# Kernel optimization log

Hardware: AMD Instinct MI355X
Metric: run time of the kernel (lower is better)

Reference implementation:

```python
import jax, jax.numpy as jnp
import numpy as np
from jax import lax

B, C, HID, H, W = 8, 256, 64, 64, 64

def conv3x3(x, w, b):
    # x: [B,C_in,H,W], w: [C_out,C_in,3,3], b: [C_out]
    y = lax.conv_general_dilated(x, w, window_strides=(1, 1), padding='SAME',
                                 dimension_numbers=('NCHW', 'OIHW', 'NCHW'))
    return y + b[None, :, None, None]

def setup_inputs() -> dict:
    key = jax.random.key(0)
    ks = jax.random.split(key, 7)
    s_in = 1.0 / np.sqrt(C * 9)
    return {
        'x': jax.random.normal(ks[0], (B, C, H, W), dtype=jnp.float32),
        'Wq': jax.random.normal(ks[1], (HID, C, 3, 3), dtype=jnp.float32) * s_in,
        'bq': jax.random.normal(ks[2], (HID,), dtype=jnp.float32) * s_in,
        'Wk': jax.random.normal(ks[3], (HID, C, 3, 3), dtype=jnp.float32) * s_in,
        'bk': jax.random.normal(ks[4], (HID,), dtype=jnp.float32) * s_in,
        'Wv': jax.random.normal(ks[5], (C, C, 3, 3), dtype=jnp.float32) * s_in,
        'bv': jax.random.normal(ks[6], (C,), dtype=jnp.float32) * s_in,
    }

def reference(x, Wq, bq, Wk, bk, Wv, bv):
    b, c, w, h = x.shape
    n = w * h
    q = conv3x3(x, Wq, bq).reshape(b, -1, n).transpose(0, 2, 1)  # [B,N,hid]
    k = conv3x3(x, Wk, bk).reshape(b, -1, n)                      # [B,hid,N]
    v = conv3x3(x, Wv, bv).reshape(b, c, n)                       # [B,C,N]
    attn = jax.nn.softmax(jnp.einsum('bnd,bdm->bnm', q, k), axis=-1)  # [B,N,N]
    # out = bmm(value, attn^T): out[b,c,m] = sum_n v[b,c,n] * attn[b,m,n]
    out = jnp.einsum('bcn,bmn->bcm', v, attn).reshape(b, c, w, h)
    # F.interpolate(out, h, mode='bilinear') with H==W is an exact identity
    return out + x
```

## Files before the change

kernel.cpp:

```cpp
#include <hip/hip_runtime.h>
#include <math.h>

#define NB   8
#define NC   256
#define ND   64
#define NPIX 4096
#define LSTR 72

typedef short bf16x8 __attribute__((ext_vector_type(8)));
typedef float f32x4  __attribute__((ext_vector_type(4)));
typedef float f32x16 __attribute__((ext_vector_type(16)));

static __device__ __forceinline__ ushort f2bf(float f) {
    uint u = __float_as_uint(f);
    u += 0x7fffu + ((u >> 16) & 1u);
    return (ushort)(u >> 16);
}
static __device__ __forceinline__ float bf2f(ushort h) {
    return __uint_as_float(((uint)h) << 16);
}

__global__ __launch_bounds__(256) void transpose_x(
    const float* __restrict__ x, ushort* __restrict__ xth, ushort* __restrict__ xtl)
{
    __shared__ float tile[64][68];
    const int t = threadIdx.x;
    const int p0 = blockIdx.x * 64, c0 = blockIdx.y * 64, b = blockIdx.z;

    const int cl = t >> 4, p4 = (t & 15) * 4;
    #pragma unroll
    for (int i = 0; i < 4; i++) {
        const int c = cl + 16 * i;
        *(float4*)&tile[c][p4] =
            *(const float4*)&x[((size_t)(b * NC + c0 + c)) * NPIX + p0 + p4];
    }
    __syncthreads();

    const int pl = t & 63, ch = t >> 6;
    float v[16];
    #pragma unroll
    for (int j = 0; j < 16; j++) v[j] = tile[ch * 16 + j][pl];
    ushort h[16], l[16];
    #pragma unroll
    for (int j = 0; j < 16; j++) {
        h[j] = f2bf(v[j]);
        l[j] = f2bf(v[j] - bf2f(h[j]));
    }
    const size_t o = ((size_t)(b * NPIX + p0 + pl)) * 256 + c0 + ch * 16;
    *(uint4*)&xth[o]     = *(uint4*)&h[0];
    *(uint4*)&xth[o + 8] = *(uint4*)&h[8];
    *(uint4*)&xtl[o]     = *(uint4*)&l[0];
    *(uint4*)&xtl[o + 8] = *(uint4*)&l[8];
}

__global__ __launch_bounds__(256) void transpose_w(
    const float* __restrict__ Wq, const float* __restrict__ Wk,
    const float* __restrict__ Wv,
    ushort* __restrict__ qh, ushort* __restrict__ ql,
    ushort* __restrict__ kh, ushort* __restrict__ kl,
    ushort* __restrict__ vh)
{
    __shared__ float wb[2304];
    const int g = blockIdx.x, t = threadIdx.x;
    const float* src;
    ushort *dh, *dl;
    int co, Co, split;
    if (g < 64)       { src = Wq + (size_t)g * 2304; co = g;       Co = 64;  dh = qh; dl = ql; split = 1; }
    else if (g < 128) { src = Wk + (size_t)(g - 64) * 2304; co = g - 64; Co = 64; dh = kh; dl = kl; split = 1; }
    else              { src = Wv + (size_t)(g - 128) * 2304; co = g - 128; Co = 256; dh = vh; dl = nullptr; split = 0; }

    for (int i = t; i < 2304; i += 256) wb[i] = src[i];
    __syncthreads();
    for (int j = t; j < 2304; j += 256) {
        const int rs = j >> 8, ci = j & 255;
        const float v = wb[ci * 9 + rs];
        const ushort hv = f2bf(v);
        const size_t o = ((size_t)(rs * Co + co)) * 256 + ci;
        dh[o] = hv;
        if (split) dl[o] = f2bf(v - bf2f(hv));
    }
}

__global__ __launch_bounds__(256) void conv_split_k(
    const ushort* __restrict__ xth, const ushort* __restrict__ xtl,
    const ushort* __restrict__ wqh, const ushort* __restrict__ wql,
    const ushort* __restrict__ wkh, const ushort* __restrict__ wkl,
    const float* __restrict__ bq, const float* __restrict__ bk,
    ushort* __restrict__ qoh, ushort* __restrict__ qol,
    ushort* __restrict__ koh, ushort* __restrict__ kol)
{
    extern __shared__ char smem[];
    ushort* xsh = (ushort*)smem;
    ushort* xsl = xsh + 6 * 66 * 24;
    ushort* wsp = xsl + 6 * 66 * 24;
    float*  sbias = (float*)(wsp + 9 * 64 * 24);

    const int hq = blockIdx.x, b = blockIdx.y, ct = blockIdx.z;
    const ushort* wth = ct ? wkh : wqh;
    const ushort* wtl = ct ? wkl : wql;
    const float*  bias = ct ? bk : bq;
    ushort* outh = ct ? koh : qoh;
    ushort* outl = ct ? kol : qol;

    const int t = threadIdx.x;
    const int wv = t >> 6, lane = t & 63;
    const int l31 = lane & 31, khl = lane >> 5;
    const int lanebase = l31 * 24 + khl * 8;
    const int h = hq * 4 + wv;

    if (t < 64) sbias[t] = bias[t];
    for (int i = t; i < 384; i += 256) {
        const int p = i / 192, r2 = i % 192;
        const int row = r2 / 32, e = (r2 % 32) / 16, ci = r2 & 15;
        (p ? xsl : xsh)[(row * 66 + e * 65) * 24 + ci] = 0;
    }

    f32x16 a00 = {0}, a01 = {0}, a10 = {0}, a11 = {0};

    for (int ch = 0; ch < 16; ch++) {
        __syncthreads();
        const int ci0 = ch * 16;
        #pragma unroll
        for (int pl2 = 0; pl2 < 2; pl2++) {
            const ushort* src = pl2 ? xtl : xth;
            ushort* dst = pl2 ? xsl : xsh;
            #pragma unroll
            for (int i = 0; i < 3; i++) {
                const int a = i * 256 + t;
                const int cih = a & 1, col = (a >> 1) & 63, row = a >> 7;
                const int hs = hq * 4 + row - 1;
                uint4 val = {0, 0, 0, 0};
                if (hs >= 0 && hs < 64)
                    val = *(const uint4*)&src[((size_t)(b * NPIX + hs * 64 + col)) * 256 + ci0 + cih * 8];
                *(uint4*)&dst[(row * 66 + 1 + col) * 24 + cih * 8] = val;
            }
        }
        #pragma unroll
        for (int i = 0; i < 5; i++) {
            const int a = i * 256 + t;
            if (a < 1152) {
                const int cih = a & 1, co = (a >> 1) & 63, rs = a >> 7;
                uint4 wv4 = *(const uint4*)&wth[((size_t)(rs * 64 + co)) * 256 + ci0 + cih * 8];
                *(uint4*)&wsp[(rs * 64 + co) * 24 + cih * 8] = wv4;
            }
        }
        __syncthreads();
        #pragma unroll
        for (int rs = 0; rs < 9; rs++) {
            const int r = rs / 3, s = rs % 3;
            bf16x8 A0 = *(const bf16x8*)&wsp[rs * 1536 + lanebase];
            bf16x8 A1 = *(const bf16x8*)&wsp[rs * 1536 + 768 + lanebase];
            const int xo = ((wv + r) * 66 + s) * 24 + lanebase;
            bf16x8 B0h = *(const bf16x8*)&xsh[xo];
            bf16x8 B1h = *(const bf16x8*)&xsh[xo + 768];
            bf16x8 B0l = *(const bf16x8*)&xsl[xo];
            bf16x8 B1l = *(const bf16x8*)&xsl[xo + 768];
            a00 = __builtin_amdgcn_mfma_f32_32x32x16_bf16(A0, B0h, a00, 0, 0, 0);
            a01 = __builtin_amdgcn_mfma_f32_32x32x16_bf16(A0, B1h, a01, 0, 0, 0);
            a10 = __builtin_amdgcn_mfma_f32_32x32x16_bf16(A1, B0h, a10, 0, 0, 0);
            a11 = __builtin_amdgcn_mfma_f32_32x32x16_bf16(A1, B1h, a11, 0, 0, 0);
            a00 = __builtin_amdgcn_mfma_f32_32x32x16_bf16(A0, B0l, a00, 0, 0, 0);
            a01 = __builtin_amdgcn_mfma_f32_32x32x16_bf16(A0, B1l, a01, 0, 0, 0);
            a10 = __builtin_amdgcn_mfma_f32_32x32x16_bf16(A1, B0l, a10, 0, 0, 0);
            a11 = __builtin_amdgcn_mfma_f32_32x32x16_bf16(A1, B1l, a11, 0, 0, 0);
        }
        __syncthreads();
        #pragma unroll
        for (int i = 0; i < 5; i++) {
            const int a = i * 256 + t;
            if (a < 1152) {
                const int cih = a & 1, co = (a >> 1) & 63, rs = a >> 7;
                uint4 wv4 = *(const uint4*)&wtl[((size_t)(rs * 64 + co)) * 256 + ci0 + cih * 8];
                *(uint4*)&wsp[(rs * 64 + co) * 24 + cih * 8] = wv4;
            }
        }
        __syncthreads();
        #pragma unroll
        for (int rs = 0; rs < 9; rs++) {
            const int r = rs / 3, s = rs % 3;
            bf16x8 A0 = *(const bf16x8*)&wsp[rs * 1536 + lanebase];
            bf16x8 A1 = *(const bf16x8*)&wsp[rs * 1536 + 768 + lanebase];
            const int xo = ((wv + r) * 66 + s) * 24 + lanebase;
            bf16x8 B0h = *(const bf16x8*)&xsh[xo];
            bf16x8 B1h = *(const bf16x8*)&xsh[xo + 768];
            a00 = __builtin_amdgcn_mfma_f32_32x32x16_bf16(A0, B0h, a00, 0, 0, 0);
            a01 = __builtin_amdgcn_mfma_f32_32x32x16_bf16(A0, B1h, a01, 0, 0, 0);
            a10 = __builtin_amdgcn_mfma_f32_32x32x16_bf16(A1, B0h, a10, 0, 0, 0);
            a11 = __builtin_amdgcn_mfma_f32_32x32x16_bf16(A1, B1h, a11, 0, 0, 0);
        }
    }

    const float4* sb4 = (const float4*)sbias;
    #pragma unroll
    for (int ms = 0; ms < 2; ms++)
        #pragma unroll
        for (int ns = 0; ns < 2; ns++) {
            const f32x16 av = ms ? (ns ? a11 : a10) : (ns ? a01 : a00);
            const int p = h * 64 + ns * 32 + l31;
            #pragma unroll
            for (int g = 0; g < 4; g++) {
                const float4 bi = sb4[ms * 8 + 2 * g + khl];
                float v0 = av[4 * g + 0] + bi.x;
                float v1 = av[4 * g + 1] + bi.y;
                float v2 = av[4 * g + 2] + bi.z;
                float v3 = av[4 * g + 3] + bi.w;
                ushort4 hv, lv;
                hv.x = f2bf(v0); lv.x = f2bf(v0 - bf2f(hv.x));
                hv.y = f2bf(v1); lv.y = f2bf(v1 - bf2f(hv.y));
                hv.z = f2bf(v2); lv.z = f2bf(v2 - bf2f(hv.z));
                hv.w = f2bf(v3); lv.w = f2bf(v3 - bf2f(hv.w));
                const size_t o = ((size_t)(b * NPIX + p)) * 64 + ms * 32 + 8 * g + 4 * khl;
                *(ushort4*)&outh[o] = hv;
                *(ushort4*)&outl[o] = lv;
            }
        }
}

__global__ __launch_bounds__(256) void conv_v_k(
    const ushort* __restrict__ xth, const ushort* __restrict__ wtv,
    const float* __restrict__ bv, ushort* __restrict__ vout)
{
    extern __shared__ char smem[];
    ushort* xsh = (ushort*)smem;
    ushort* wsp = xsh + 6 * 66 * 24;
    float*  sbias = (float*)(wsp + 9 * 64 * 24);

    const int hq = blockIdx.x, b = blockIdx.y, co0 = blockIdx.z * 64;
    const int t = threadIdx.x;
    const int wv = t >> 6, lane = t & 63;
    const int l31 = lane & 31, khl = lane >> 5;
    const int lanebase = l31 * 24 + khl * 8;
    const int h = hq * 4 + wv;

    if (t < 64) sbias[t] = bv[co0 + t];
    for (int i = t; i < 192; i += 256) {
        const int row = i / 32, e = (i % 32) / 16, ci = i & 15;
        xsh[(row * 66 + e * 65) * 24 + ci] = 0;
    }

    f32x16 a00 = {0}, a01 = {0}, a10 = {0}, a11 = {0};

    for (int ch = 0; ch < 16; ch++) {
        __syncthreads();
        const int ci0 = ch * 16;
        #pragma unroll
        for (int i = 0; i < 3; i++) {
            const int a = i * 256 + t;
            const int cih = a & 1, col = (a >> 1) & 63, row = a >> 7;
            const int hs = hq * 4 + row - 1;
            uint4 val = {0, 0, 0, 0};
            if (hs >= 0 && hs < 64)
                val = *(const uint4*)&xth[((size_t)(b * NPIX + hs * 64 + col)) * 256 + ci0 + cih * 8];
            *(uint4*)&xsh[(row * 66 + 1 + col) * 24 + cih * 8] = val;
        }
        #pragma unroll
        for (int i = 0; i < 5; i++) {
            const int a = i * 256 + t;
            if (a < 1152) {
                const int cih = a & 1, co = (a >> 1) & 63, rs = a >> 7;
                uint4 wv4 = *(const uint4*)&wtv[((size_t)(rs * 256 + co0 + co)) * 256 + ci0 + cih * 8];
                *(uint4*)&wsp[(rs * 64 + co) * 24 + cih * 8] = wv4;
            }
        }
        __syncthreads();
        #pragma unroll
        for (int rs = 0; rs < 9; rs++) {
            const int r = rs / 3, s = rs % 3;
            const int xo = ((wv + r) * 66 + s) * 24 + lanebase;
            bf16x8 A0 = *(const bf16x8*)&xsh[xo];
            bf16x8 A1 = *(const bf16x8*)&xsh[xo + 768];
            bf16x8 B0 = *(const bf16x8*)&wsp[rs * 1536 + lanebase];
            bf16x8 B1 = *(const bf16x8*)&wsp[rs * 1536 + 768 + lanebase];
            a00 = __builtin_amdgcn_mfma_f32_32x32x16_bf16(A0, B0, a00, 0, 0, 0);
            a01 = __builtin_amdgcn_mfma_f32_32x32x16_bf16(A0, B1, a01, 0, 0, 0);
            a10 = __builtin_amdgcn_mfma_f32_32x32x16_bf16(A1, B0, a10, 0, 0, 0);
            a11 = __builtin_amdgcn_mfma_f32_32x32x16_bf16(A1, B1, a11, 0, 0, 0);
        }
    }

    #pragma unroll
    for (int ns = 0; ns < 2; ns++) {
        const int co = co0 + ns * 32 + l31;
        const float bi = sbias[ns * 32 + l31];
        #pragma unroll
        for (int ms = 0; ms < 2; ms++) {
            const f32x16 av = ms ? (ns ? a11 : a10) : (ns ? a01 : a00);
            #pragma unroll
            for (int g = 0; g < 4; g++) {
                const int p = h * 64 + ms * 32 + 8 * g + 4 * khl;
                ushort4 ov;
                ov.x = f2bf(av[4 * g + 0] + bi);
                ov.y = f2bf(av[4 * g + 1] + bi);
                ov.z = f2bf(av[4 * g + 2] + bi);
                ov.w = f2bf(av[4 * g + 3] + bi);
                *(ushort4*)&vout[((size_t)(b * NC + co)) * NPIX + p] = ov;
            }
        }
    }
}

__global__ __launch_bounds__(256, 2) void attn_k(
    const ushort* __restrict__ qh, const ushort* __restrict__ ql,
    const ushort* __restrict__ kh, const ushort* __restrict__ kl,
    const ushort* __restrict__ vb, const float* __restrict__ x,
    float* __restrict__ out)
{
    const int b    = blockIdx.y;
    const int m0   = blockIdx.x * 64;
    const int t    = threadIdx.x;
    const int wave = t >> 6;
    const int lane = t & 63;
    const int quad = lane >> 4;
    const int l16  = lane & 15;

    __shared__ __align__(16) char smem[65792];
    ushort* sqh = (ushort*)(smem);
    ushort* sql = (ushort*)(smem + 9216);
    ushort* skh = (ushort*)(smem + 18432);
    ushort* skl = (ushort*)(smem + 27648);
    ushort* svs = (ushort*)(smem + 18432);
    ushort* sps = (ushort*)(smem + 55296);
    float*  red = (float*)(smem + 64512);
    float*  ivl = (float*)(smem + 65536);

    {
        const int r = t >> 2, dc = (t & 3) * 16;
        const size_t g = ((size_t)b * NPIX + m0 + r) * ND + dc;
        uint4 a0 = *(const uint4*)&qh[g];
        uint4 a1 = *(const uint4*)&qh[g + 8];
        *(uint4*)&sqh[r * LSTR + dc]     = a0;
        *(uint4*)&sqh[r * LSTR + dc + 8] = a1;
        uint4 b0 = *(const uint4*)&ql[g];
        uint4 b1 = *(const uint4*)&ql[g + 8];
        *(uint4*)&sql[r * LSTR + dc]     = b0;
        *(uint4*)&sql[r * LSTR + dc + 8] = b1;
    }

    f32x4 acc[16];
    #pragma unroll
    for (int i = 0; i < 16; i++) acc[i] = (f32x4){0.f, 0.f, 0.f, 0.f};
    float rsum = 0.f;
    const int rs_row = t & 63, rs_c = (t >> 6) * 16;

    for (int n0 = 0; n0 < NPIX; n0 += 64) {
        __syncthreads();
        {
            const int r = t >> 2, dc = (t & 3) * 16;
            const size_t g = ((size_t)b * NPIX + n0 + r) * ND + dc;
            uint4 a0 = *(const uint4*)&kh[g];
            uint4 a1 = *(const uint4*)&kh[g + 8];
            *(uint4*)&skh[r * LSTR + dc]     = a0;
            *(uint4*)&skh[r * LSTR + dc + 8] = a1;
            uint4 b0 = *(const uint4*)&kl[g];
            uint4 b1 = *(const uint4*)&kl[g + 8];
            *(uint4*)&skl[r * LSTR + dc]     = b0;
            *(uint4*)&skl[r * LSTR + dc + 8] = b1;
        }
        __syncthreads();

        bf16x8 aqh[2], aql[2];
        const int am = 16 * wave + l16;
        #pragma unroll
        for (int ks = 0; ks < 2; ks++) {
            aqh[ks] = *(const bf16x8*)&sqh[am * LSTR + ks * 32 + quad * 8];
            aql[ks] = *(const bf16x8*)&sql[am * LSTR + ks * 32 + quad * 8];
        }
        #pragma unroll
        for (int nt = 0; nt < 4; nt++) {
            f32x4 s = {0.f, 0.f, 0.f, 0.f};
            const int bn = nt * 16 + l16;
            #pragma unroll
            for (int ks = 0; ks < 2; ks++) {
                bf16x8 bh = *(const bf16x8*)&skh[bn * LSTR + ks * 32 + quad * 8];
                bf16x8 bl = *(const bf16x8*)&skl[bn * LSTR + ks * 32 + quad * 8];
                s = __builtin_amdgcn_mfma_f32_16x16x32_bf16(aqh[ks], bh, s, 0, 0, 0);
                s = __builtin_amdgcn_mfma_f32_16x16x32_bf16(aql[ks], bh, s, 0, 0, 0);
                s = __builtin_amdgcn_mfma_f32_16x16x32_bf16(aqh[ks], bl, s, 0, 0, 0);
            }
            #pragma unroll
            for (int r = 0; r < 4; r++) {
                float p = __expf(s[r] - 30.f);
                sps[(16 * wave + quad * 4 + r) * LSTR + nt * 16 + l16] = f2bf(p);
            }
        }
        __syncthreads();

        {
            const int c0 = t >> 2, ncs = (t & 3) * 16;
            #pragma unroll
            for (int cc = 0; cc < 4; cc++) {
                const int c = cc * 64 + c0;
                const size_t g = ((size_t)b * NC + c) * NPIX + n0 + ncs;
                uint4 a0 = *(const uint4*)&vb[g];
                uint4 a1 = *(const uint4*)&vb[g + 8];
                *(uint4*)&svs[c * LSTR + ncs]     = a0;
                *(uint4*)&svs[c * LSTR + ncs + 8] = a1;
            }
            uint4 p0 = *(const uint4*)&sps[rs_row * LSTR + rs_c];
            uint4 p1 = *(const uint4*)&sps[rs_row * LSTR + rs_c + 8];
            const ushort* pu0 = (const ushort*)&p0;
            const ushort* pu1 = (const ushort*)&p1;
            float ss = 0.f;
            #pragma unroll
            for (int i = 0; i < 8; i++) ss += bf2f(pu0[i]) + bf2f(pu1[i]);
            rsum += ss;
        }
        __syncthreads();

        bf16x8 ap[4][2];
        #pragma unroll
        for (int ms = 0; ms < 4; ms++)
            #pragma unroll
            for (int ks = 0; ks < 2; ks++)
                ap[ms][ks] = *(const bf16x8*)&sps[(16 * ms + l16) * LSTR + ks * 32 + quad * 8];
        #pragma unroll
        for (int ct = 0; ct < 4; ct++) {
            const int c = 64 * wave + ct * 16 + l16;
            #pragma unroll
            for (int ks = 0; ks < 2; ks++) {
                bf16x8 bv = *(const bf16x8*)&svs[c * LSTR + ks * 32 + quad * 8];
                #pragma unroll
                for (int ms = 0; ms < 4; ms++)
                    acc[ms * 4 + ct] = __builtin_amdgcn_mfma_f32_16x16x32_bf16(
                        ap[ms][ks], bv, acc[ms * 4 + ct], 0, 0, 0);
            }
        }
    }

    red[(t & 63) * 4 + (t >> 6)] = rsum;
    __syncthreads();
    if (t < 64)
        ivl[t] = 1.f / (red[t * 4 + 0] + red[t * 4 + 1] + red[t * 4 + 2] + red[t * 4 + 3]);
    __syncthreads();

    #pragma unroll
    for (int ms = 0; ms < 4; ms++) {
        const float il0 = ivl[16 * ms + quad * 4 + 0];
        const float il1 = ivl[16 * ms + quad * 4 + 1];
        const float il2 = ivl[16 * ms + quad * 4 + 2];
        const float il3 = ivl[16 * ms + quad * 4 + 3];
        const int m = m0 + 16 * ms + quad * 4;
        #pragma unroll
        for (int ct = 0; ct < 4; ct++) {
            const int c = 64 * wave + ct * 16 + l16;
            const size_t base = ((size_t)b * NC + c) * NPIX + m;
            float4 xv = *(const float4*)&x[base];
            f32x4 a = acc[ms * 4 + ct];
            float4 o;
            o.x = fmaf(a[0], il0, xv.x);
            o.y = fmaf(a[1], il1, xv.y);
            o.z = fmaf(a[2], il2, xv.z);
            o.w = fmaf(a[3], il3, xv.w);
            *(float4*)&out[base] = o;
        }
    }
}

extern "C" void kernel_launch(void* const* d_in, const int* in_sizes, int n_in,
                              void* d_out, int out_size, void* d_ws, size_t ws_size,
                              hipStream_t stream)
{
    const float* x  = (const float*)d_in[0];
    const float* Wq = (const float*)d_in[1];
    const float* bq = (const float*)d_in[2];
    const float* Wk = (const float*)d_in[3];
    const float* bk = (const float*)d_in[4];
    const float* Wv = (const float*)d_in[5];
    const float* bv = (const float*)d_in[6];
    float* outp = (float*)d_out;

    const size_t XT = (size_t)NB * NPIX * 256;
    const size_t QK = (size_t)NB * NPIX * ND;
    ushort* xt_h = (ushort*)d_ws;
    ushort* xt_l = xt_h + XT;
    ushort* v_b  = xt_l;
    ushort* q_h  = xt_l + XT;
    ushort* q_l  = q_h + QK;
    ushort* k_h  = q_l + QK;
    ushort* k_l  = k_h + QK;
    ushort* wtq_h = k_l + QK;
    ushort* wtq_l = wtq_h + 147456;
    ushort* wtk_h = wtq_l + 147456;
    ushort* wtk_l = wtk_h + 147456;
    ushort* wtv_h = wtk_l + 147456;

    dim3 blk(256);
    transpose_x<<<dim3(64, 4, NB), blk, 0, stream>>>(x, xt_h, xt_l);
    transpose_w<<<dim3(384), blk, 0, stream>>>(Wq, Wk, Wv, wtq_h, wtq_l, wtk_h, wtk_l, wtv_h);
    conv_split_k<<<dim3(16, NB, 2), blk, 65920, stream>>>(
        xt_h, xt_l, wtq_h, wtq_l, wtk_h, wtk_l, bq, bk, q_h, q_l, k_h, k_l);
    conv_v_k<<<dim3(16, NB, 4), blk, 46912, stream>>>(xt_h, wtv_h, bv, v_b);
    attn_k<<<dim3(64, NB), blk, 0, stream>>>(q_h, q_l, k_h, k_l, v_b, x, outp);
}
```

Measured before the change: 427.8 us.

## Double-buffer conv inputs, read weights from global, and retile attention to 512 threads

The two conv kernels now keep a double-buffered LDS tile of the input. The next channel chunk is prefetched into registers while the current one is computed, and weights are read straight from global memory instead of being staged in LDS, which drops several barriers per chunk. The QK conv also merges its separate low-weight pass into one loop over the three hi/lo MFMA products. The attention kernel moves to 512 threads and 128 query rows per block, keeps Q in registers, double-buffers K in LDS, and loads V fragments directly from global memory without staging them. The trade-offs are more register pressure and uncoalesced global weight and V reads in exchange for fewer synchronisations and more overlap.

```diff
diff --git a/kernel.cpp b/kernel.cpp
--- a/kernel.cpp
+++ b/kernel.cpp
@@ -81,7 +81,7 @@
     }
 }
 
-__global__ __launch_bounds__(256) void conv_split_k(
+__global__ __launch_bounds__(256) void conv_qk_k(
     const ushort* __restrict__ xth, const ushort* __restrict__ xtl,
     const ushort* __restrict__ wqh, const ushort* __restrict__ wql,
     const ushort* __restrict__ wkh, const ushort* __restrict__ wkl,
@@ -90,10 +90,8 @@
     ushort* __restrict__ koh, ushort* __restrict__ kol)
 {
     extern __shared__ char smem[];
-    ushort* xsh = (ushort*)smem;
-    ushort* xsl = xsh + 6 * 66 * 24;
-    ushort* wsp = xsl + 6 * 66 * 24;
-    float*  sbias = (float*)(wsp + 9 * 64 * 24);
+    ushort* xs = (ushort*)smem;
+    float*  sbias = (float*)(smem + 76032);
 
     const int hq = blockIdx.x, b = blockIdx.y, ct = blockIdx.z;
     const ushort* wth = ct ? wkh : wqh;
@@ -109,85 +107,94 @@
     const int h = hq * 4 + wv;
 
     if (t < 64) sbias[t] = bias[t];
-    for (int i = t; i < 384; i += 256) {
-        const int p = i / 192, r2 = i % 192;
+    for (int i = t; i < 768; i += 256) {
+        const int buf = i / 384, rem = i % 384;
+        const int p = rem / 192, r2 = rem % 192;
         const int row = r2 / 32, e = (r2 % 32) / 16, ci = r2 & 15;
-        (p ? xsl : xsh)[(row * 66 + e * 65) * 24 + ci] = 0;
-    }
+        xs[(size_t)(buf * 2 + p) * 9504 + (row * 66 + e * 65) * 24 + ci] = 0;
+    }
+
+    int s_cih[3], s_col[3], s_row[3], s_hs[3];
+    #pragma unroll
+    for (int i = 0; i < 3; i++) {
+        const int a = i * 256 + t;
+        s_cih[i] = a & 1; s_col[i] = (a >> 1) & 63; s_row[i] = a >> 7;
+        s_hs[i] = hq * 4 + s_row[i] - 1;
+    }
+
+    uint4 xr[6];
+    #pragma unroll
+    for (int i = 0; i < 3; i++) {
+        uint4 vh = {0,0,0,0}, vl = {0,0,0,0};
+        if (s_hs[i] >= 0 && s_hs[i] < 64) {
+            const size_t g = ((size_t)(b * NPIX + s_hs[i] * 64 + s_col[i])) * 256 + s_cih[i] * 8;
+            vh = *(const uint4*)&xth[g];
+            vl = *(const uint4*)&xtl[g];
+        }
+        xr[i] = vh; xr[3 + i] = vl;
+    }
+    #pragma unroll
+    for (int i = 0; i < 3; i++) {
+        const size_t o = (s_row[i] * 66 + 1 + s_col[i]) * 24 + s_cih[i] * 8;
+        *(uint4*)&xs[o]                   = xr[i];
+        *(uint4*)&xs[(size_t)9504 + o]    = xr[3 + i];
+    }
+    __syncthreads();
 
     f32x16 a00 = {0}, a01 = {0}, a10 = {0}, a11 = {0};
 
     for (int ch = 0; ch < 16; ch++) {
-        __syncthreads();
-        const int ci0 = ch * 16;
-        #pragma unroll
-        for (int pl2 = 0; pl2 < 2; pl2++) {
-            const ushort* src = pl2 ? xtl : xth;
-            ushort* dst = pl2 ? xsl : xsh;
+        const int cur = ch & 1, ci0 = ch * 16;
+        if (ch < 15) {
+            const int ci1 = ci0 + 16;
             #pragma unroll
             for (int i = 0; i < 3; i++) {
-                const int a = i * 256 + t;
-                const int cih = a & 1, col = (a >> 1) & 63, row = a >> 7;
-                const int hs = hq * 4 + row - 1;
-                uint4 val = {0, 0, 0, 0};
-                if (hs >= 0 && hs < 64)
-                    val = *(const uint4*)&src[((size_t)(b * NPIX + hs * 64 + col)) * 256 + ci0 + cih * 8];
-                *(uint4*)&dst[(row * 66 + 1 + col) * 24 + cih * 8] = val;
-            }
-        }
-        #pragma unroll
-        for (int i = 0; i < 5; i++) {
-            const int a = i * 256 + t;
-            if (a < 1152) {
-                const int cih = a & 1, co = (a >> 1) & 63, rs = a >> 7;
-                uint4 wv4 = *(const uint4*)&wth[((size_t)(rs * 64 + co)) * 256 + ci0 + cih * 8];
-                *(uint4*)&wsp[(rs * 64 + co) * 24 + cih * 8] = wv4;
-            }
-        }
-        __syncthreads();
+                uint4 vh = {0,0,0,0}, vl = {0,0,0,0};
+                if (s_hs[i] >= 0 && s_hs[i] < 64) {
+                    const size_t g = ((size_t)(b * NPIX + s_hs[i] * 64 + s_col[i])) * 256 + ci1 + s_cih[i] * 8;
+                    vh = *(const uint4*)&xth[g];
+                    vl = *(const uint4*)&xtl[g];
+                }
+                xr[i] = vh; xr[3 + i] = vl;
+            }
+        }
+        const ushort* xh = xs + (size_t)(cur * 2 + 0) * 9504;
+        const ushort* xl = xs + (size_t)(cur * 2 + 1) * 9504;
         #pragma unroll
         for (int rs = 0; rs < 9; rs++) {
             const int r = rs / 3, s = rs % 3;
-            bf16x8 A0 = *(const bf16x8*)&wsp[rs * 1536 + lanebase];
-            bf16x8 A1 = *(const bf16x8*)&wsp[rs * 1536 + 768 + lanebase];
+            bf16x8 A0h = *(const bf16x8*)&wth[((size_t)(rs * 64 + l31)) * 256 + ci0 + khl * 8];
+            bf16x8 A1h = *(const bf16x8*)&wth[((size_t)(rs * 64 + 32 + l31)) * 256 + ci0 + khl * 8];
+            bf16x8 A0l = *(const bf16x8*)&wtl[((size_t)(rs * 64 + l31)) * 256 + ci0 + khl * 8];
+            bf16x8 A1l = *(const bf16x8*)&wtl[((size_t)(rs * 64 + 32 + l31)) * 256 + ci0 + khl * 8];
             const int xo = ((wv + r) * 66 + s) * 24 + lanebase;
-            bf16x8 B0h = *(const bf16x8*)&xsh[xo];
-            bf16x8 B1h = *(const bf16x8*)&xsh[xo + 768];
-            bf16x8 B0l = *(const bf16x8*)&xsl[xo];
-            bf16x8 B1l = *(const bf16x8*)&xsl[xo + 768];
-            a00 = __builtin_amdgcn_mfma_f32_32x32x16_bf16(A0, B0h, a00, 0, 0, 0);
-            a01 = __builtin_amdgcn_mfma_f32_32x32x16_bf16(A0, B1h, a01, 0, 0, 0);
-            a10 = __builtin_amdgcn_mfma_f32_32x32x16_bf16(A1, B0h, a10, 0, 0, 0);
-            a11 = __builtin_amdgcn_mfma_f32_32x32x16_bf16(A1, B1h, a11, 0, 0, 0);
-            a00 = __builtin_amdgcn_mfma_f32_32x32x16_bf16(A0, B0l, a00, 0, 0, 0);
-            a01 = __builtin_amdgcn_mfma_f32_32x32x16_bf16(A0, B1l, a01, 0, 0, 0);
-            a10 = __builtin_amdgcn_mfma_f32_32x32x16_bf16(A1, B0l, a10, 0, 0, 0);
-            a11 = __builtin_amdgcn_mfma_f32_32x32x16_bf16(A1, B1l, a11, 0, 0, 0);
+            bf16x8 B0h = *(const bf16x8*)&xh[xo];
+            bf16x8 B1h = *(const bf16x8*)&xh[xo + 768];
+            bf16x8 B0l = *(const bf16x8*)&xl[xo];
+            bf16x8 B1l = *(const bf16x8*)&xl[xo + 768];
+            a00 = __builtin_amdgcn_mfma_f32_32x32x16_bf16(A0h, B0h, a00, 0, 0, 0);
+            a01 = __builtin_amdgcn_mfma_f32_32x32x16_bf16(A0h, B1h, a01, 0, 0, 0);
+            a10 = __builtin_amdgcn_mfma_f32_32x32x16_bf16(A1h, B0h, a10, 0, 0, 0);
+            a11 = __builtin_amdgcn_mfma_f32_32x32x16_bf16(A1h, B1h, a11, 0, 0, 0);
+            a00 = __builtin_amdgcn_mfma_f32_32x32x16_bf16(A0l, B0h, a00, 0, 0, 0);
+            a01 = __builtin_amdgcn_mfma_f32_32x32x16_bf16(A0l, B1h, a01, 0, 0, 0);
+            a10 = __builtin_amdgcn_mfma_f32_32x32x16_bf16(A1l, B0h, a10, 0, 0, 0);
+            a11 = __builtin_amdgcn_mfma_f32_32x32x16_bf16(A1l, B1h, a11, 0, 0, 0);
+            a00 = __builtin_amdgcn_mfma_f32_32x32x16_bf16(A0h, B0l, a00, 0, 0, 0);
+            a01 = __builtin_amdgcn_mfma_f32_32x32x16_bf16(A0h, B1l, a01, 0, 0, 0);
+            a10 = __builtin_amdgcn_mfma_f32_32x32x16_bf16(A1h, B0l, a10, 0, 0, 0);
+            a11 = __builtin_amdgcn_mfma_f32_32x32x16_bf16(A1h, B1l, a11, 0, 0, 0);
+        }
+        if (ch < 15) {
+            const int nb = cur ^ 1;
+            #pragma unroll
+            for (int i = 0; i < 3; i++) {
+                const size_t o = (size_t)(nb * 2) * 9504 + (s_row[i] * 66 + 1 + s_col[i]) * 24 + s_cih[i] * 8;
+                *(uint4*)&xs[o]        = xr[i];
+                *(uint4*)&xs[o + 9504] = xr[3 + i];
+            }
         }
         __syncthreads();
-        #pragma unroll
-        for (int i = 0; i < 5; i++) {
-            const int a = i * 256 + t;
-            if (a < 1152) {
-                const int cih = a & 1, co = (a >> 1) & 63, rs = a >> 7;
-                uint4 wv4 = *(const uint4*)&wtl[((size_t)(rs * 64 + co)) * 256 + ci0 + cih * 8];
-                *(uint4*)&wsp[(rs * 64 + co) * 24 + cih * 8] = wv4;
-            }
-        }
-        __syncthreads();
-        #pragma unroll
-        for (int rs = 0; rs < 9; rs++) {
-            const int r = rs / 3, s = rs % 3;
-            bf16x8 A0 = *(const bf16x8*)&wsp[rs * 1536 + lanebase];
-            bf16x8 A1 = *(const bf16x8*)&wsp[rs * 1536 + 768 + lanebase];
-            const int xo = ((wv + r) * 66 + s) * 24 + lanebase;
-            bf16x8 B0h = *(const bf16x8*)&xsh[xo];
-            bf16x8 B1h = *(const bf16x8*)&xsh[xo + 768];
-            a00 = __builtin_amdgcn_mfma_f32_32x32x16_bf16(A0, B0h, a00, 0, 0, 0);
-            a01 = __builtin_amdgcn_mfma_f32_32x32x16_bf16(A0, B1h, a01, 0, 0, 0);
-            a10 = __builtin_amdgcn_mfma_f32_32x32x16_bf16(A1, B0h, a10, 0, 0, 0);
-            a11 = __builtin_amdgcn_mfma_f32_32x32x16_bf16(A1, B1h, a11, 0, 0, 0);
-        }
     }
 
     const float4* sb4 = (const float4*)sbias;
@@ -221,9 +228,8 @@
     const float* __restrict__ bv, ushort* __restrict__ vout)
 {
     extern __shared__ char smem[];
-    ushort* xsh = (ushort*)smem;
-    ushort* wsp = xsh + 6 * 66 * 24;
-    float*  sbias = (float*)(wsp + 9 * 64 * 24);
+    ushort* xs = (ushort*)smem;
+    float*  sbias = (float*)(smem + 38016);
 
     const int hq = blockIdx.x, b = blockIdx.y, co0 = blockIdx.z * 64;
     const int t = threadIdx.x;
@@ -233,49 +239,68 @@
     const int h = hq * 4 + wv;
 
     if (t < 64) sbias[t] = bv[co0 + t];
-    for (int i = t; i < 192; i += 256) {
-        const int row = i / 32, e = (i % 32) / 16, ci = i & 15;
-        xsh[(row * 66 + e * 65) * 24 + ci] = 0;
-    }
+    for (int i = t; i < 384; i += 256) {
+        const int buf = i / 192, r2 = i % 192;
+        const int row = r2 / 32, e = (r2 % 32) / 16, ci = r2 & 15;
+        xs[(size_t)buf * 9504 + (row * 66 + e * 65) * 24 + ci] = 0;
+    }
+
+    int s_cih[3], s_col[3], s_row[3], s_hs[3];
+    #pragma unroll
+    for (int i = 0; i < 3; i++) {
+        const int a = i * 256 + t;
+        s_cih[i] = a & 1; s_col[i] = (a >> 1) & 63; s_row[i] = a >> 7;
+        s_hs[i] = hq * 4 + s_row[i] - 1;
+    }
+
+    uint4 xr[3];
+    #pragma unroll
+    for (int i = 0; i < 3; i++) {
+        uint4 vh = {0,0,0,0};
+        if (s_hs[i] >= 0 && s_hs[i] < 64)
+            vh = *(const uint4*)&xth[((size_t)(b * NPIX + s_hs[i] * 64 + s_col[i])) * 256 + s_cih[i] * 8];
+        xr[i] = vh;
+    }
+    #pragma unroll
+    for (int i = 0; i < 3; i++)
+        *(uint4*)&xs[(s_row[i] * 66 + 1 + s_col[i]) * 24 + s_cih[i] * 8] = xr[i];
+    __syncthreads();
 
     f32x16 a00 = {0}, a01 = {0}, a10 = {0}, a11 = {0};
 
     for (int ch = 0; ch < 16; ch++) {
-        __syncthreads();
-        const int ci0 = ch * 16;
-        #pragma unroll
-        for (int i = 0; i < 3; i++) {
-            const int a = i * 256 + t;
-            const int cih = a & 1, col = (a >> 1) & 63, row = a >> 7;
-            const int hs = hq * 4 + row - 1;
-            uint4 val = {0, 0, 0, 0};
-            if (hs >= 0 && hs < 64)
-                val = *(const uint4*)&xth[((size_t)(b * NPIX + hs * 64 + col)) * 256 + ci0 + cih * 8];
-            *(uint4*)&xsh[(row * 66 + 1 + col) * 24 + cih * 8] = val;
-        }
-        #pragma unroll
-        for (int i = 0; i < 5; i++) {
-            const int a = i * 256 + t;
-            if (a < 1152) {
-                const int cih = a & 1, co = (a >> 1) & 63, rs = a >> 7;
-                uint4 wv4 = *(const uint4*)&wtv[((size_t)(rs * 256 + co0 + co)) * 256 + ci0 + cih * 8];
-                *(uint4*)&wsp[(rs * 64 + co) * 24 + cih * 8] = wv4;
-            }
-        }
-        __syncthreads();
+        const int cur = ch & 1, ci0 = ch * 16;
+        if (ch < 15) {
+            const int ci1 = ci0 + 16;
+            #pragma unroll
+            for (int i = 0; i < 3; i++) {
+                uint4 vh = {0,0,0,0};
+                if (s_hs[i] >= 0 && s_hs[i] < 64)
+                    vh = *(const uint4*)&xth[((size_t)(b * NPIX + s_hs[i] * 64 + s_col[i])) * 256 + ci1 + s_cih[i] * 8];
+                xr[i] = vh;
+            }
+        }
+        const ushort* xh = xs + (size_t)cur * 9504;
         #pragma unroll
         for (int rs = 0; rs < 9; rs++) {
             const int r = rs / 3, s = rs % 3;
             const int xo = ((wv + r) * 66 + s) * 24 + lanebase;
-            bf16x8 A0 = *(const bf16x8*)&xsh[xo];
-            bf16x8 A1 = *(const bf16x8*)&xsh[xo + 768];
-            bf16x8 B0 = *(const bf16x8*)&wsp[rs * 1536 + lanebase];
-            bf16x8 B1 = *(const bf16x8*)&wsp[rs * 1536 + 768 + lanebase];
+            bf16x8 A0 = *(const bf16x8*)&xh[xo];
+            bf16x8 A1 = *(const bf16x8*)&xh[xo + 768];
+            bf16x8 B0 = *(const bf16x8*)&wtv[((size_t)(rs * 256 + co0 + l31)) * 256 + ci0 + khl * 8];
+            bf16x8 B1 = *(const bf16x8*)&wtv[((size_t)(rs * 256 + co0 + 32 + l31)) * 256 + ci0 + khl * 8];
             a00 = __builtin_amdgcn_mfma_f32_32x32x16_bf16(A0, B0, a00, 0, 0, 0);
             a01 = __builtin_amdgcn_mfma_f32_32x32x16_bf16(A0, B1, a01, 0, 0, 0);
             a10 = __builtin_amdgcn_mfma_f32_32x32x16_bf16(A1, B0, a10, 0, 0, 0);
             a11 = __builtin_amdgcn_mfma_f32_32x32x16_bf16(A1, B1, a11, 0, 0, 0);
         }
+        if (ch < 15) {
+            const int nb = cur ^ 1;
+            #pragma unroll
+            for (int i = 0; i < 3; i++)
+                *(uint4*)&xs[(size_t)nb * 9504 + (s_row[i] * 66 + 1 + s_col[i]) * 24 + s_cih[i] * 8] = xr[i];
+        }
+        __syncthreads();
     }
 
     #pragma unroll
@@ -299,105 +324,109 @@
     }
 }
 
-__global__ __launch_bounds__(256, 2) void attn_k(
+__global__ __launch_bounds__(512, 2) void attn_k(
     const ushort* __restrict__ qh, const ushort* __restrict__ ql,
     const ushort* __restrict__ kh, const ushort* __restrict__ kl,
     const ushort* __restrict__ vb, const float* __restrict__ x,
     float* __restrict__ out)
 {
     const int b    = blockIdx.y;
-    const int m0   = blockIdx.x * 64;
+    const int m0   = blockIdx.x * 128;
     const int t    = threadIdx.x;
     const int wave = t >> 6;
     const int lane = t & 63;
     const int quad = lane >> 4;
     const int l16  = lane & 15;
 
-    __shared__ __align__(16) char smem[65792];
-    ushort* sqh = (ushort*)(smem);
-    ushort* sql = (ushort*)(smem + 9216);
-    ushort* skh = (ushort*)(smem + 18432);
-    ushort* skl = (ushort*)(smem + 27648);
-    ushort* svs = (ushort*)(smem + 18432);
-    ushort* sps = (ushort*)(smem + 55296);
-    float*  red = (float*)(smem + 64512);
-    float*  ivl = (float*)(smem + 65536);
-
+    extern __shared__ char smem[];
+    ushort* skh = (ushort*)(smem);
+    ushort* skl = (ushort*)(smem + 18432);
+    ushort* sps = (ushort*)(smem + 36864);
+    float*  red = (float*)(smem + 55296);
+    float*  ivl = (float*)(smem + 57344);
+
+    const int mgbase = 2 * (wave & 3);
+    const int ntbase = 2 * (wave >> 2);
+    bf16x8 aqh[2][2], aql[2][2];
+    #pragma unroll
+    for (int mgi = 0; mgi < 2; mgi++)
+        #pragma unroll
+        for (int ks = 0; ks < 2; ks++) {
+            const size_t g = ((size_t)b * NPIX + m0 + 16 * (mgbase + mgi) + l16) * ND + 32 * ks + quad * 8;
+            aqh[mgi][ks] = *(const bf16x8*)&qh[g];
+            aql[mgi][ks] = *(const bf16x8*)&ql[g];
+        }
+
+    const int krow = t >> 3, kseg = (t & 7) * 8;
     {
-        const int r = t >> 2, dc = (t & 3) * 16;
-        const size_t g = ((size_t)b * NPIX + m0 + r) * ND + dc;
-        uint4 a0 = *(const uint4*)&qh[g];
-        uint4 a1 = *(const uint4*)&qh[g + 8];
-        *(uint4*)&sqh[r * LSTR + dc]     = a0;
-        *(uint4*)&sqh[r * LSTR + dc + 8] = a1;
-        uint4 b0 = *(const uint4*)&ql[g];
-        uint4 b1 = *(const uint4*)&ql[g + 8];
-        *(uint4*)&sql[r * LSTR + dc]     = b0;
-        *(uint4*)&sql[r * LSTR + dc + 8] = b1;
-    }
-
-    f32x4 acc[16];
-    #pragma unroll
-    for (int i = 0; i < 16; i++) acc[i] = (f32x4){0.f, 0.f, 0.f, 0.f};
+        const size_t g = ((size_t)b * NPIX + krow) * ND + kseg;
+        *(uint4*)&skh[krow * LSTR + kseg] = *(const uint4*)&kh[g];
+        *(uint4*)&skl[krow * LSTR + kseg] = *(const uint4*)&kl[g];
+    }
+
+    f32x4 acc[8][2];
+    #pragma unroll
+    for (int i = 0; i < 8; i++)
+        #pragma unroll
+        for (int j = 0; j < 2; j++) acc[i][j] = (f32x4){0.f, 0.f, 0.f, 0.f};
     float rsum = 0.f;
-    const int rs_row = t & 63, rs_c = (t >> 6) * 16;
+    const int rs_row = t & 127, rs_co = (t >> 7) * 16;
+    __syncthreads();
 
     for (int n0 = 0; n0 < NPIX; n0 += 64) {
+        const int cur = (n0 >> 6) & 1, nxt = cur ^ 1;
+
+        bf16x8 vf[2][2];
+        #pragma unroll
+        for (int ct = 0; ct < 2; ct++)
+            #pragma unroll
+            for (int ks = 0; ks < 2; ks++) {
+                const int c = 32 * wave + 16 * ct + l16;
+                vf[ct][ks] = *(const bf16x8*)&vb[((size_t)b * NC + c) * NPIX + n0 + 32 * ks + quad * 8];
+            }
+        uint4 knh = {0,0,0,0}, knl = {0,0,0,0};
+        const bool have_next = (n0 + 64) < NPIX;
+        if (have_next) {
+            const size_t g = ((size_t)b * NPIX + n0 + 64 + krow) * ND + kseg;
+            knh = *(const uint4*)&kh[g];
+            knl = *(const uint4*)&kl[g];
+        }
+
+        #pragma unroll
+        for (int nti = 0; nti < 2; nti++) {
+            const int nt = ntbase + nti;
+            bf16x8 bh[2], bl[2];
+            #pragma unroll
+            for (int ks = 0; ks < 2; ks++) {
+                const int o = cur * 4608 + (16 * nt + l16) * LSTR + 32 * ks + quad * 8;
+                bh[ks] = *(const bf16x8*)&skh[o];
+                bl[ks] = *(const bf16x8*)&skl[o];
+            }
+            #pragma unroll
+            for (int mgi = 0; mgi < 2; mgi++) {
+                f32x4 s = {0.f, 0.f, 0.f, 0.f};
+                #pragma unroll
+                for (int ks = 0; ks < 2; ks++) {
+                    s = __builtin_amdgcn_mfma_f32_16x16x32_bf16(aqh[mgi][ks], bh[ks], s, 0, 0, 0);
+                    s = __builtin_amdgcn_mfma_f32_16x16x32_bf16(aql[mgi][ks], bh[ks], s, 0, 0, 0);
+                    s = __builtin_amdgcn_mfma_f32_16x16x32_bf16(aqh[mgi][ks], bl[ks], s, 0, 0, 0);
+                }
+                #pragma unroll
+                for (int r = 0; r < 4; r++) {
+                    const float p = __expf(s[r] - 30.f);
+                    sps[(16 * (mgbase + mgi) + quad * 4 + r) * LSTR + 16 * nt + l16] = f2bf(p);
+                }
+            }
+        }
+        if (have_next) {
+            *(uint4*)&skh[nxt * 4608 + krow * LSTR + kseg] = knh;
+            *(uint4*)&skl[nxt * 4608 + krow * LSTR + kseg] = knl;
+        }
         __syncthreads();
+
         {
-            const int r = t >> 2, dc = (t & 3) * 16;
-            const size_t g = ((size_t)b * NPIX + n0 + r) * ND + dc;
-            uint4 a0 = *(const uint4*)&kh[g];
-            uint4 a1 = *(const uint4*)&kh[g + 8];
-            *(uint4*)&skh[r * LSTR + dc]     = a0;
-            *(uint4*)&skh[r * LSTR + dc + 8] = a1;
-            uint4 b0 = *(const uint4*)&kl[g];
-            uint4 b1 = *(const uint4*)&kl[g + 8];
-            *(uint4*)&skl[r * LSTR + dc]     = b0;
-            *(uint4*)&skl[r * LSTR + dc + 8] = b1;
-        }
-        __syncthreads();
-
-        bf16x8 aqh[2], aql[2];
-        const int am = 16 * wave + l16;
-        #pragma unroll
-        for (int ks = 0; ks < 2; ks++) {
-            aqh[ks] = *(const bf16x8*)&sqh[am * LSTR + ks * 32 + quad * 8];
-            aql[ks] = *(const bf16x8*)&sql[am * LSTR + ks * 32 + quad * 8];
-        }
-        #pragma unroll
-        for (int nt = 0; nt < 4; nt++) {
-            f32x4 s = {0.f, 0.f, 0.f, 0.f};
-            const int bn = nt * 16 + l16;
-            #pragma unroll
-            for (int ks = 0; ks < 2; ks++) {
-                bf16x8 bh = *(const bf16x8*)&skh[bn * LSTR + ks * 32 + quad * 8];
-                bf16x8 bl = *(const bf16x8*)&skl[bn * LSTR + ks * 32 + quad * 8];
-                s = __builtin_amdgcn_mfma_f32_16x16x32_bf16(aqh[ks], bh, s, 0, 0, 0);
-                s = __builtin_amdgcn_mfma_f32_16x16x32_bf16(aql[ks], bh, s, 0, 0, 0);
-                s = __builtin_amdgcn_mfma_f32_16x16x32_bf16(aqh[ks], bl, s, 0, 0, 0);
-            }
-            #pragma unroll
-            for (int r = 0; r < 4; r++) {
-                float p = __expf(s[r] - 30.f);
-                sps[(16 * wave + quad * 4 + r) * LSTR + nt * 16 + l16] = f2bf(p);
-            }
-        }
-        __syncthreads();
-
-        {
-            const int c0 = t >> 2, ncs = (t & 3) * 16;
-            #pragma unroll
-            for (int cc = 0; cc < 4; cc++) {
-                const int c = cc * 64 + c0;
-                const size_t g = ((size_t)b * NC + c) * NPIX + n0 + ncs;
-                uint4 a0 = *(const uint4*)&vb[g];
-                uint4 a1 = *(const uint4*)&vb[g + 8];
-                *(uint4*)&svs[c * LSTR + ncs]     = a0;
-                *(uint4*)&svs[c * LSTR + ncs + 8] = a1;
-            }
-            uint4 p0 = *(const uint4*)&sps[rs_row * LSTR + rs_c];
-            uint4 p1 = *(const uint4*)&sps[rs_row * LSTR + rs_c + 8];
+            uint4 p0 = *(const uint4*)&sps[rs_row * LSTR + rs_co];
+            uint4 p1 = *(const uint4*)&sps[rs_row * LSTR + rs_co + 8];
             const ushort* pu0 = (const ushort*)&p0;
             const ushort* pu1 = (const ushort*)&p1;
             float ss = 0.f;
@@ -405,52 +434,45 @@
             for (int i = 0; i < 8; i++) ss += bf2f(pu0[i]) + bf2f(pu1[i]);
             rsum += ss;
         }
+
+        #pragma unroll
+        for (int ks = 0; ks < 2; ks++) {
+            bf16x8 ap[8];
+            #pragma unroll
+            for (int mg = 0; mg < 8; mg++)
+                ap[mg] = *(const bf16x8*)&sps[(16 * mg + l16) * LSTR + 32 * ks + quad * 8];
+            #pragma unroll
+            for (int mg = 0; mg < 8; mg++)
+                #pragma unroll
+                for (int ct = 0; ct < 2; ct++)
+                    acc[mg][ct] = __builtin_amdgcn_mfma_f32_16x16x32_bf16(
+                        ap[mg], vf[ct][ks], acc[mg][ct], 0, 0, 0);
+        }
         __syncthreads();
-
-        bf16x8 ap[4][2];
-        #pragma unroll
-        for (int ms = 0; ms < 4; ms++)
-            #pragma unroll
-            for (int ks = 0; ks < 2; ks++)
-                ap[ms][ks] = *(const bf16x8*)&sps[(16 * ms + l16) * LSTR + ks * 32 + quad * 8];
-        #pragma unroll
-        for (int ct = 0; ct < 4; ct++) {
-            const int c = 64 * wave + ct * 16 + l16;
-            #pragma unroll
-            for (int ks = 0; ks < 2; ks++) {
-                bf16x8 bv = *(const bf16x8*)&svs[c * LSTR + ks * 32 + quad * 8];
-                #pragma unroll
-                for (int ms = 0; ms < 4; ms++)
-                    acc[ms * 4 + ct] = __builtin_amdgcn_mfma_f32_16x16x32_bf16(
-                        ap[ms][ks], bv, acc[ms * 4 + ct], 0, 0, 0);
-            }
-        }
-    }
-
-    red[(t & 63) * 4 + (t >> 6)] = rsum;
-    __syncthreads();
-    if (t < 64)
+    }
+
+    red[rs_row * 4 + (t >> 7)] = rsum;
+    __syncthreads();
+    if (t < 128)
         ivl[t] = 1.f / (red[t * 4 + 0] + red[t * 4 + 1] + red[t * 4 + 2] + red[t * 4 + 3]);
     __syncthreads();
 
     #pragma unroll
-    for (int ms = 0; ms < 4; ms++) {
-        const float il0 = ivl[16 * ms + quad * 4 + 0];
-        const float il1 = ivl[16 * ms + quad * 4 + 1];
-        const float il2 = ivl[16 * ms + quad * 4 + 2];
-        const float il3 = ivl[16 * ms + quad * 4 + 3];
-        const int m = m0 + 16 * ms + quad * 4;
-        #pragma unroll
-        for (int ct = 0; ct < 4; ct++) {
-            const int c = 64 * wave + ct * 16 + l16;
+    for (int mg = 0; mg < 8; mg++) {
+        const int mrow = 16 * mg + quad * 4;
+        const float4 il4 = *(const float4*)&ivl[mrow];
+        const int m = m0 + mrow;
+        #pragma unroll
+        for (int ct = 0; ct < 2; ct++) {
+            const int c = 32 * wave + 16 * ct + l16;
             const size_t base = ((size_t)b * NC + c) * NPIX + m;
-            float4 xv = *(const float4*)&x[base];
-            f32x4 a = acc[ms * 4 + ct];
+            const float4 xv = *(const float4*)&x[base];
+            const f32x4 a = acc[mg][ct];
             float4 o;
-            o.x = fmaf(a[0], il0, xv.x);
-            o.y = fmaf(a[1], il1, xv.y);
-            o.z = fmaf(a[2], il2, xv.z);
-            o.w = fmaf(a[3], il3, xv.w);
+            o.x = fmaf(a[0], il4.x, xv.x);
+            o.y = fmaf(a[1], il4.y, xv.y);
+            o.z = fmaf(a[2], il4.z, xv.z);
+            o.w = fmaf(a[3], il4.w, xv.w);
             *(float4*)&out[base] = o;
         }
     }
@@ -487,8 +509,8 @@
     dim3 blk(256);
     transpose_x<<<dim3(64, 4, NB), blk, 0, stream>>>(x, xt_h, xt_l);
     transpose_w<<<dim3(384), blk, 0, stream>>>(Wq, Wk, Wv, wtq_h, wtq_l, wtk_h, wtk_l, wtv_h);
-    conv_split_k<<<dim3(16, NB, 2), blk, 65920, stream>>>(
+    conv_qk_k<<<dim3(16, NB, 2), blk, 76288, stream>>>(
         xt_h, xt_l, wtq_h, wtq_l, wtk_h, wtk_l, bq, bk, q_h, q_l, k_h, k_l);
-    conv_v_k<<<dim3(16, NB, 4), blk, 46912, stream>>>(xt_h, wtv_h, bv, v_b);
-    attn_k<<<dim3(64, NB), blk, 0, stream>>>(q_h, q_l, k_h, k_l, v_b, x, outp);
-}
+    conv_v_k<<<dim3(16, NB, 4), blk, 38272, stream>>>(xt_h, wtv_h, bv, v_b);
+    attn_k<<<dim3(32, NB), dim3(512), 57856, stream>>>(q_h, q_l, k_h, k_l, v_b, x, outp);
+}
```

After: 438.0 us. 1.02x slower.
